# Performance work log

Hardware: AMD Instinct MI355X
Metric: run time of the kernel (lower is better)

The kernel has to match this reference:

```python
import jax, jax.numpy as jnp
import numpy as np

IN_CH = 12
STEP = 4
UPLAG = 2048
HIDDEN = 1024
OUTPUT = 256
BATCH = 2048
FEAT = UPLAG // STEP  # per-channel conv output length


def setup_inputs() -> dict:
    key = jax.random.key(0)
    ks = jax.random.split(key, 7)
    s = 1.0 / np.sqrt(STEP)
    x = jax.random.normal(ks[0], (BATCH, IN_CH, UPLAG), dtype=jnp.float32)
    # per-channel Conv1d(1,1,step,step) weights/biases, stacked: [C, step], [C]
    W1 = jax.random.uniform(ks[1], (IN_CH, STEP), jnp.float32, -s, s)
    b1 = jax.random.uniform(ks[2], (IN_CH,), jnp.float32, -s, s)
    d_in = IN_CH * FEAT
    s2 = 1.0 / np.sqrt(d_in)
    W2 = jax.random.uniform(ks[3], (d_in, HIDDEN), jnp.float32, -s2, s2)
    b2 = jax.random.uniform(ks[4], (HIDDEN,), jnp.float32, -s2, s2)
    s3 = 1.0 / np.sqrt(HIDDEN)
    W3 = jax.random.uniform(ks[5], (HIDDEN, OUTPUT), jnp.float32, -s3, s3)
    b3 = jax.random.uniform(ks[6], (OUTPUT,), jnp.float32, -s3, s3)
    return {"x": x, "W1": W1, "b1": b1, "W2": W2, "b2": b2, "W3": W3, "b3": b3}


def reference(x, W1, b1, W2, b2, W3, b3):
    B, C, L = x.shape
    # Non-overlapping patch reduction equivalent to Conv1d(1,1,step,step) per channel:
    # view [B, C, F, step], contract step dim against per-channel kernel.
    xp = x.reshape(B, C, L // STEP, STEP)
    conv = jnp.einsum('bcfk,ck->bcf', xp, W1) + b1[None, :, None]  # [B, C, F]
    flat = conv.reshape(B, C * (L // STEP))  # concat order: channel-major, matches torch.cat
    h = jax.nn.relu(flat @ W2 + b2)
    out = h @ W3 + b3
    return out.reshape(B, 1, -1)
```

## Files before the change

kernel.cpp:

```cpp
#include <hip/hip_runtime.h>
#include <hip/hip_bf16.h>

#define BATCH   2048
#define IN_CH   12
#define UPLAG   2048
#define STEP    4
#define FEAT    512
#define DIN     6144
#define HIDDEN  1024
#define OUTPUT  256

typedef __bf16 bf16x8 __attribute__((ext_vector_type(8)));
typedef float  f32x4  __attribute__((ext_vector_type(4)));

__device__ __forceinline__ unsigned short f2bf(float f) {
  unsigned int u = __builtin_bit_cast(unsigned int, f);
  unsigned int r = (u + 0x7fffu + ((u >> 16) & 1u)) >> 16;
  return (unsigned short)r;
}

__device__ __forceinline__ float bf2f(unsigned short h) {
  unsigned int u = ((unsigned int)h) << 16;
  return __builtin_bit_cast(float, u);
}

__device__ __forceinline__ void async_copy16(const unsigned short* g, unsigned short* l) {
  __builtin_amdgcn_global_load_lds(
      (const __attribute__((address_space(1))) unsigned int*)g,
      (__attribute__((address_space(3))) unsigned int*)l, 16, 0, 0);
}

#define CONV_BLOCKS 4096
#define W2T_BLOCKS  1536
#define W3T_BLOCKS  64

__global__ __launch_bounds__(256) void prep_kernel(
    const float* __restrict__ x, const float* __restrict__ W1,
    const float* __restrict__ b1, unsigned short* __restrict__ flatA,
    const float* __restrict__ W2, unsigned short* __restrict__ W2T,
    const float* __restrict__ W3, unsigned short* __restrict__ W3T)
{
  __shared__ float tile[64][65];
  const int t = threadIdx.x;
  int b = blockIdx.x;

  if (b < CONV_BLOCKS) {
    const int total = BATCH * DIN;
    for (int gid = b * 256 + t; gid < total; gid += CONV_BLOCKS * 256) {
      int cf = gid % DIN;
      int c  = cf >> 9;
      float4 xv = ((const float4*)x)[gid];
      float4 wv = ((const float4*)W1)[c];
      float v = xv.x * wv.x + xv.y * wv.y + xv.z * wv.z + xv.w * wv.w + b1[c];
      flatA[gid] = f2bf(v);
    }
    return;
  }

  const float* in; unsigned short* outp; int R, Ncol, bx, by;
  if (b < CONV_BLOCKS + W2T_BLOCKS) {
    int idx = b - CONV_BLOCKS;
    in = W2; outp = W2T; R = DIN; Ncol = HIDDEN;
    bx = (idx & 15) * 64; by = (idx >> 4) * 64;
  } else {
    int idx = b - CONV_BLOCKS - W2T_BLOCKS;
    in = W3; outp = W3T; R = HIDDEN; Ncol = OUTPUT;
    bx = (idx & 3) * 64; by = (idx >> 2) * 64;
  }
  int tx = t & 63, ty = t >> 6;
  #pragma unroll
  for (int i = 0; i < 64; i += 4)
    tile[ty + i][tx] = in[(size_t)(by + ty + i) * Ncol + bx + tx];
  __syncthreads();
  #pragma unroll
  for (int i = 0; i < 64; i += 4)
    outp[(size_t)(bx + ty + i) * R + by + tx] = f2bf(tile[tx][ty + i]);
}

#define G1_BM 128
#define G1_BN 128
#define G1_BK 64
#define SPLITK 6

__global__ __launch_bounds__(256, 2) void gemm1_kernel(
    const unsigned short* __restrict__ A,
    const unsigned short* __restrict__ BT,
    unsigned short* __restrict__ Cp,
    int M, int N, int K)
{
  __shared__ unsigned short As[G1_BM * G1_BK];
  __shared__ unsigned short Bs[G1_BN * G1_BK];
  const int t    = threadIdx.x;
  const int lane = t & 63;
  const int wave = t >> 6;

  int b    = blockIdx.x;
  int xcdg = b & 7;
  int rest = b >> 3;
  int xt   = rest & 7;
  int zz   = rest >> 3;
  int zt   = zz >> 1;
  int yt   = (xcdg << 1) | (zz & 1);

  const int m0 = yt * G1_BM;
  const int n0 = xt * G1_BN;
  const int Ks = K / SPLITK;
  const int kbeg = zt * Ks;

  const int wm = (wave >> 1) * 64;
  const int wn = (wave & 1) * 64;
  const int lm = lane & 15;
  const int kgrp = lane >> 4;

  f32x4 acc[4][4];
  #pragma unroll
  for (int i = 0; i < 4; i++)
    #pragma unroll
    for (int j = 0; j < 4; j++) {
      f32x4 z = {0.f, 0.f, 0.f, 0.f};
      acc[i][j] = z;
    }

  const unsigned short* Ag = A  + (size_t)m0 * K + kbeg;
  const unsigned short* Bg = BT + (size_t)n0 * K + kbeg;

  for (int kk = 0; kk < Ks; kk += G1_BK) {
    #pragma unroll
    for (int r = 0; r < 4; ++r) {
      int c = r * 256 + t;
      int row = c >> 3;
      int gk  = (c & 7) ^ (row & 7);
      async_copy16(Ag + (size_t)row * K + kk + gk * 8, As + c * 8);
    }
    #pragma unroll
    for (int r = 0; r < 4; ++r) {
      int c = r * 256 + t;
      int row = c >> 3;
      int gk  = (c & 7) ^ (row & 7);
      async_copy16(Bg + (size_t)row * K + kk + gk * 8, Bs + c * 8);
    }
    __syncthreads();

    #pragma unroll
    for (int s = 0; s < 2; ++s) {
      const int kch = kgrp + s * 4;
      bf16x8 af[4], bfr[4];
      #pragma unroll
      for (int i = 0; i < 4; i++) {
        int row = wm + i * 16 + lm;
        af[i] = *(const bf16x8*)(As + row * G1_BK + ((kch ^ (row & 7)) * 8));
      }
      #pragma unroll
      for (int j = 0; j < 4; j++) {
        int row = wn + j * 16 + lm;
        bfr[j] = *(const bf16x8*)(Bs + row * G1_BK + ((kch ^ (row & 7)) * 8));
      }
      #pragma unroll
      for (int i = 0; i < 4; i++)
        #pragma unroll
        for (int j = 0; j < 4; j++)
          acc[i][j] = __builtin_amdgcn_mfma_f32_16x16x32_bf16(af[i], bfr[j], acc[i][j], 0, 0, 0);
    }
    __syncthreads();
  }

  unsigned short* Co = Cp + (size_t)zt * M * N;
  const int rbase = kgrp * 4;
  #pragma unroll
  for (int i = 0; i < 4; i++)
    #pragma unroll
    for (int j = 0; j < 4; j++) {
      int col = n0 + wn + j * 16 + lm;
      #pragma unroll
      for (int r = 0; r < 4; r++) {
        int row = m0 + wm + i * 16 + rbase + r;
        Co[(size_t)row * N + col] = f2bf(acc[i][j][r]);
      }
    }
}

#define TB_M 16
#define HS_STRIDE (HIDDEN + 8)

__global__ __launch_bounds__(256) void tail_kernel(
    const unsigned short* __restrict__ Cp,
    const float* __restrict__ b2,
    const unsigned short* __restrict__ W3T,
    const float* __restrict__ b3,
    float* __restrict__ out)
{
  __shared__ unsigned short hs[TB_M * HS_STRIDE];
  const int t = threadIdx.x;
  const int lane = t & 63;
  const int wave = t >> 6;
  const int m0 = blockIdx.x * TB_M;
  const int MN = BATCH * HIDDEN;

  for (int idx = t; idx < TB_M * (HIDDEN / 4); idx += 256) {
    int r  = idx >> 8;
    int c4 = idx & 255;
    size_t base = (size_t)(m0 + r) * HIDDEN + c4 * 4;
    float4 s = *(const float4*)(b2 + c4 * 4);
    #pragma unroll
    for (int p = 0; p < SPLITK; ++p) {
      ushort4 a = *(const ushort4*)(Cp + (size_t)p * MN + base);
      s.x += bf2f(a.x); s.y += bf2f(a.y); s.z += bf2f(a.z); s.w += bf2f(a.w);
    }
    ushort4 o;
    o.x = f2bf(fmaxf(s.x, 0.f));
    o.y = f2bf(fmaxf(s.y, 0.f));
    o.z = f2bf(fmaxf(s.z, 0.f));
    o.w = f2bf(fmaxf(s.w, 0.f));
    *(ushort4*)(hs + r * HS_STRIDE + c4 * 4) = o;
  }
  __syncthreads();

  const int lm = lane & 15;
  const int kgrp = lane >> 4;
  const int ncol0 = wave * 64;
  f32x4 acc[4];
  #pragma unroll
  for (int j = 0; j < 4; j++) {
    f32x4 z = {0.f, 0.f, 0.f, 0.f};
    acc[j] = z;
  }

  #pragma unroll 2
  for (int kk = 0; kk < HIDDEN; kk += 32) {
    bf16x8 af = *(const bf16x8*)(hs + lm * HS_STRIDE + kk + kgrp * 8);
    #pragma unroll
    for (int j = 0; j < 4; j++) {
      const unsigned short* bp =
          W3T + (size_t)(ncol0 + j * 16 + lm) * HIDDEN + kk + kgrp * 8;
      bf16x8 bfr = *(const bf16x8*)bp;
      acc[j] = __builtin_amdgcn_mfma_f32_16x16x32_bf16(af, bfr, acc[j], 0, 0, 0);
    }
  }

  const int rbase = kgrp * 4;
  #pragma unroll
  for (int j = 0; j < 4; j++) {
    int col = ncol0 + j * 16 + lm;
    float bias = b3[col];
    #pragma unroll
    for (int r = 0; r < 4; r++) {
      int row = m0 + rbase + r;
      out[(size_t)row * OUTPUT + col] = acc[j][r] + bias;
    }
  }
}

extern "C" void kernel_launch(void* const* d_in, const int* in_sizes, int n_in,
                              void* d_out, int out_size, void* d_ws, size_t ws_size,
                              hipStream_t stream)
{
  const float* x  = (const float*)d_in[0];
  const float* W1 = (const float*)d_in[1];
  const float* b1 = (const float*)d_in[2];
  const float* W2 = (const float*)d_in[3];
  const float* b2 = (const float*)d_in[4];
  const float* W3 = (const float*)d_in[5];
  const float* b3 = (const float*)d_in[6];
  float* out = (float*)d_out;

  char* ws = (char*)d_ws;
  unsigned short* flatA = (unsigned short*)ws; ws += (size_t)BATCH * DIN * 2;
  unsigned short* W2T   = (unsigned short*)ws; ws += (size_t)HIDDEN * DIN * 2;
  unsigned short* W3T   = (unsigned short*)ws; ws += (size_t)OUTPUT * HIDDEN * 2;
  unsigned short* Cpart = (unsigned short*)ws; ws += (size_t)SPLITK * BATCH * HIDDEN * 2;

  prep_kernel<<<CONV_BLOCKS + W2T_BLOCKS + W3T_BLOCKS, 256, 0, stream>>>(
      x, W1, b1, flatA, W2, W2T, W3, W3T);
  gemm1_kernel<<<768, 256, 0, stream>>>(flatA, W2T, Cpart, BATCH, HIDDEN, DIN);
  tail_kernel<<<BATCH / TB_M, 256, 0, stream>>>(Cpart, b2, W3T, b3, out);
}
```

Before: 365.4 us.

## Halve GEMM1 K-tile, pack split-K partials in row-group layout, split tail over N

Reduces the GEMM1 K tile from 64 to 32 and drops the XOR swizzle on LDS staging. The split-K partial outputs are now stored as packed ushort4 groups of four rows, replacing the previous scalar strided stores. The tail kernel reads that packed layout and launches twice as many blocks, each covering half of the output columns. The smaller K tile doubles the number of barrier iterations and may bring back LDS bank conflicts, and the tail now recomputes the split-K reduction once per half.

```diff
diff --git a/kernel.cpp b/kernel.cpp
--- a/kernel.cpp
+++ b/kernel.cpp
@@ -79,8 +79,9 @@
 
 #define G1_BM 128
 #define G1_BN 128
-#define G1_BK 64
+#define G1_BK 32
 #define SPLITK 6
+#define MN1 (BATCH * HIDDEN)
 
 __global__ __launch_bounds__(256, 2) void gemm1_kernel(
     const unsigned short* __restrict__ A,
@@ -111,6 +112,7 @@
   const int wn = (wave & 1) * 64;
   const int lm = lane & 15;
   const int kgrp = lane >> 4;
+  const int lk = kgrp * 8;
 
   f32x4 acc[4][4];
   #pragma unroll
@@ -126,57 +128,52 @@
 
   for (int kk = 0; kk < Ks; kk += G1_BK) {
     #pragma unroll
-    for (int r = 0; r < 4; ++r) {
-      int c = r * 256 + t;
-      int row = c >> 3;
-      int gk  = (c & 7) ^ (row & 7);
-      async_copy16(Ag + (size_t)row * K + kk + gk * 8, As + c * 8);
-    }
-    #pragma unroll
-    for (int r = 0; r < 4; ++r) {
-      int c = r * 256 + t;
-      int row = c >> 3;
-      int gk  = (c & 7) ^ (row & 7);
-      async_copy16(Bg + (size_t)row * K + kk + gk * 8, Bs + c * 8);
+    for (int r = 0; r < 2; ++r) {
+      int chunk = r * 256 + t;
+      int row = chunk >> 2;
+      int kc  = (chunk & 3) * 8;
+      async_copy16(Ag + (size_t)row * K + kk + kc, As + chunk * 8);
+    }
+    #pragma unroll
+    for (int r = 0; r < 2; ++r) {
+      int chunk = r * 256 + t;
+      int row = chunk >> 2;
+      int kc  = (chunk & 3) * 8;
+      async_copy16(Bg + (size_t)row * K + kk + kc, Bs + chunk * 8);
     }
     __syncthreads();
 
-    #pragma unroll
-    for (int s = 0; s < 2; ++s) {
-      const int kch = kgrp + s * 4;
-      bf16x8 af[4], bfr[4];
+    bf16x8 af[4], bfr[4];
+    #pragma unroll
+    for (int i = 0; i < 4; i++)
+      af[i] = *(const bf16x8*)(As + (wm + i * 16 + lm) * G1_BK + lk);
+    #pragma unroll
+    for (int j = 0; j < 4; j++)
+      bfr[j] = *(const bf16x8*)(Bs + (wn + j * 16 + lm) * G1_BK + lk);
+    #pragma unroll
+    for (int i = 0; i < 4; i++)
       #pragma unroll
-      for (int i = 0; i < 4; i++) {
-        int row = wm + i * 16 + lm;
-        af[i] = *(const bf16x8*)(As + row * G1_BK + ((kch ^ (row & 7)) * 8));
-      }
-      #pragma unroll
-      for (int j = 0; j < 4; j++) {
-        int row = wn + j * 16 + lm;
-        bfr[j] = *(const bf16x8*)(Bs + row * G1_BK + ((kch ^ (row & 7)) * 8));
-      }
-      #pragma unroll
-      for (int i = 0; i < 4; i++)
-        #pragma unroll
-        for (int j = 0; j < 4; j++)
-          acc[i][j] = __builtin_amdgcn_mfma_f32_16x16x32_bf16(af[i], bfr[j], acc[i][j], 0, 0, 0);
-    }
+      for (int j = 0; j < 4; j++)
+        acc[i][j] = __builtin_amdgcn_mfma_f32_16x16x32_bf16(af[i], bfr[j], acc[i][j], 0, 0, 0);
     __syncthreads();
   }
 
-  unsigned short* Co = Cp + (size_t)zt * M * N;
-  const int rbase = kgrp * 4;
-  #pragma unroll
-  for (int i = 0; i < 4; i++)
+  unsigned short* Co = Cp + (size_t)zt * MN1;
+  const int rgbase = (m0 + wm) >> 2;
+  #pragma unroll
+  for (int i = 0; i < 4; i++) {
+    int rg = rgbase + i * 4 + kgrp;
     #pragma unroll
     for (int j = 0; j < 4; j++) {
       int col = n0 + wn + j * 16 + lm;
-      #pragma unroll
-      for (int r = 0; r < 4; r++) {
-        int row = m0 + wm + i * 16 + rbase + r;
-        Co[(size_t)row * N + col] = f2bf(acc[i][j][r]);
-      }
-    }
+      ushort4 o;
+      o.x = f2bf(acc[i][j][0]);
+      o.y = f2bf(acc[i][j][1]);
+      o.z = f2bf(acc[i][j][2]);
+      o.w = f2bf(acc[i][j][3]);
+      *(ushort4*)(Co + ((size_t)rg * HIDDEN + col) * 4) = o;
+    }
+  }
 }
 
 #define TB_M 16
@@ -189,47 +186,50 @@
     const float* __restrict__ b3,
     float* __restrict__ out)
 {
-  __shared__ unsigned short hs[TB_M * HS_STRIDE];
+  __shared__ unsigned short hs[TB_M][HS_STRIDE];
   const int t = threadIdx.x;
   const int lane = t & 63;
   const int wave = t >> 6;
-  const int m0 = blockIdx.x * TB_M;
-  const int MN = BATCH * HIDDEN;
-
-  for (int idx = t; idx < TB_M * (HIDDEN / 4); idx += 256) {
-    int r  = idx >> 8;
-    int c4 = idx & 255;
-    size_t base = (size_t)(m0 + r) * HIDDEN + c4 * 4;
-    float4 s = *(const float4*)(b2 + c4 * 4);
+  const int bi = blockIdx.x >> 1;
+  const int nh = blockIdx.x & 1;
+  const int m0 = bi * TB_M;
+  const int rg0 = m0 >> 2;
+
+  #pragma unroll
+  for (int it = 0; it < 16; ++it) {
+    int slot = it * 256 + t;
+    int rgl = slot >> 10;
+    int col = slot & (HIDDEN - 1);
+    const unsigned short* p0 = Cp + ((size_t)(rg0 + rgl) * HIDDEN + col) * 4;
+    float4 s = {0.f, 0.f, 0.f, 0.f};
     #pragma unroll
     for (int p = 0; p < SPLITK; ++p) {
-      ushort4 a = *(const ushort4*)(Cp + (size_t)p * MN + base);
+      ushort4 a = *(const ushort4*)(p0 + (size_t)p * MN1);
       s.x += bf2f(a.x); s.y += bf2f(a.y); s.z += bf2f(a.z); s.w += bf2f(a.w);
     }
-    ushort4 o;
-    o.x = f2bf(fmaxf(s.x, 0.f));
-    o.y = f2bf(fmaxf(s.y, 0.f));
-    o.z = f2bf(fmaxf(s.z, 0.f));
-    o.w = f2bf(fmaxf(s.w, 0.f));
-    *(ushort4*)(hs + r * HS_STRIDE + c4 * 4) = o;
+    float bb = b2[col];
+    hs[rgl * 4 + 0][col] = f2bf(fmaxf(s.x + bb, 0.f));
+    hs[rgl * 4 + 1][col] = f2bf(fmaxf(s.y + bb, 0.f));
+    hs[rgl * 4 + 2][col] = f2bf(fmaxf(s.z + bb, 0.f));
+    hs[rgl * 4 + 3][col] = f2bf(fmaxf(s.w + bb, 0.f));
   }
   __syncthreads();
 
   const int lm = lane & 15;
   const int kgrp = lane >> 4;
-  const int ncol0 = wave * 64;
-  f32x4 acc[4];
-  #pragma unroll
-  for (int j = 0; j < 4; j++) {
+  const int ncol0 = nh * 128 + wave * 32;
+  f32x4 acc[2];
+  #pragma unroll
+  for (int j = 0; j < 2; j++) {
     f32x4 z = {0.f, 0.f, 0.f, 0.f};
     acc[j] = z;
   }
 
-  #pragma unroll 2
+  #pragma unroll 4
   for (int kk = 0; kk < HIDDEN; kk += 32) {
-    bf16x8 af = *(const bf16x8*)(hs + lm * HS_STRIDE + kk + kgrp * 8);
-    #pragma unroll
-    for (int j = 0; j < 4; j++) {
+    bf16x8 af = *(const bf16x8*)(&hs[lm][kk + kgrp * 8]);
+    #pragma unroll
+    for (int j = 0; j < 2; j++) {
       const unsigned short* bp =
           W3T + (size_t)(ncol0 + j * 16 + lm) * HIDDEN + kk + kgrp * 8;
       bf16x8 bfr = *(const bf16x8*)bp;
@@ -237,14 +237,13 @@
     }
   }
 
-  const int rbase = kgrp * 4;
-  #pragma unroll
-  for (int j = 0; j < 4; j++) {
+  #pragma unroll
+  for (int j = 0; j < 2; j++) {
     int col = ncol0 + j * 16 + lm;
     float bias = b3[col];
     #pragma unroll
     for (int r = 0; r < 4; r++) {
-      int row = m0 + rbase + r;
+      int row = m0 + kgrp * 4 + r;
       out[(size_t)row * OUTPUT + col] = acc[j][r] + bias;
     }
   }
@@ -267,10 +266,10 @@
   unsigned short* flatA = (unsigned short*)ws; ws += (size_t)BATCH * DIN * 2;
   unsigned short* W2T   = (unsigned short*)ws; ws += (size_t)HIDDEN * DIN * 2;
   unsigned short* W3T   = (unsigned short*)ws; ws += (size_t)OUTPUT * HIDDEN * 2;
-  unsigned short* Cpart = (unsigned short*)ws; ws += (size_t)SPLITK * BATCH * HIDDEN * 2;
+  unsigned short* Cpart = (unsigned short*)ws; ws += (size_t)SPLITK * MN1 * 2;
 
   prep_kernel<<<CONV_BLOCKS + W2T_BLOCKS + W3T_BLOCKS, 256, 0, stream>>>(
       x, W1, b1, flatA, W2, W2T, W3, W3T);
   gemm1_kernel<<<768, 256, 0, stream>>>(flatA, W2T, Cpart, BATCH, HIDDEN, DIN);
-  tail_kernel<<<BATCH / TB_M, 256, 0, stream>>>(Cpart, b2, W3T, b3, out);
-}
+  tail_kernel<<<2 * (BATCH / TB_M), 256, 0, stream>>>(Cpart, b2, W3T, b3, out);
+}
```

Measured after the change: 359.9 us. About the same (-1.5%).
